# Performance work log

Measured on AMD Instinct MI355X. Metric: run time of the kernel, lower is better.

## Reference

```python
import jax, jax.numpy as jnp
import numpy as np
from jax import lax

BN_EPS = 1e-5


def _conv1d(h, w, b=None):
    # h: [B, Cin, L], w: [Cout, Cin, K], 'same' padding for odd K
    k = w.shape[-1]
    out = lax.conv_general_dilated(h, w, (1,), [(k // 2, k // 2)],
                                   dimension_numbers=('NCH', 'OIH', 'NCH'))
    if b is not None:
        out = out + b[None, :, None]
    return out


def _bn(h, gamma, beta):
    # eval-mode BatchNorm1d with running_mean=0, running_var=1
    return h * (gamma[None, :, None] / jnp.sqrt(1.0 + BN_EPS)) + beta[None, :, None]


def _encoder(h, cw, cb, rw, gammas, betas, aw, au):
    # h: [B, D, L] -> V: [B, C, F]
    t = jnp.tanh(_conv1d(h, cw, cb))
    t = _bn(t, gammas[0], betas[0])
    for i in range(rw.shape[0]):  # residual blocks
        t = jnp.tanh(_bn(_conv1d(t, rw[i]), gammas[i + 1], betas[i + 1]) + t)
    # label attention: w [A,F], u [C,A]
    Z = jnp.tanh(jnp.einsum('af,bfl->bal', aw, t))
    A = jax.nn.softmax(jnp.einsum('ca,bal->bcl', au, Z), axis=2)
    V = jnp.einsum('bfl,bcl->bcf', t, A)
    return V


def setup_inputs() -> dict:
    key = jax.random.key(0)
    ks = list(jax.random.split(key, 32))
    B, L, D, C, VOC, NE, N, E = 16, 4096, 256, 50, 50000, 20050, 512, 8192
    F, A, FFN = 100, 256, 128

    def rn(k, shape, s):
        return (jax.random.normal(k, shape, jnp.float32) * s).astype(jnp.float32)

    x = jax.random.randint(ks[0], (B, L), 0, VOC)
    attention_mask = jnp.ones((B, L), jnp.int32)
    nodes = jax.random.randint(ks[1], (B, N), 0, NE)
    src = jax.random.randint(ks[2], (B, E), 0, N)
    off = jax.random.randint(ks[3], (B, E), 1, N)
    dst = (src + off) % N  # guaranteed no self-loops
    edges = jnp.stack([src, dst], axis=1)  # [B, 2, E]

    inp = dict(x=x, attention_mask=attention_mask, nodes=nodes, edges=edges)
    inp['word_emb'] = rn(ks[4], (VOC, D), 0.02)
    inp['entity_emb'] = rn(ks[5], (NE, D), 0.02)
    i = 6
    for ksz in (3, 5, 9):
        inp[f'convw{ksz}'] = rn(ks[i], (F, D, ksz), (2.0 / (D * ksz)) ** 0.5); i += 1
        inp[f'convb{ksz}'] = jnp.zeros((F,), jnp.float32)
        inp[f'resw{ksz}'] = rn(ks[i], (2, F, F, ksz), (2.0 / (F * ksz)) ** 0.5); i += 1
    inp['bn_gamma'] = jnp.ones((3, 3, F), jnp.float32)
    inp['bn_beta'] = jnp.zeros((3, 3, F), jnp.float32)
    inp['attn_w'] = rn(ks[i], (3, A, F), 0.05); i += 1
    inp['attn_u'] = rn(ks[i], (3, C, A), 0.05); i += 1
    inp['gc1_w'] = rn(ks[i], (D, D), (1.0 / D) ** 0.5); i += 1
    inp['gc1_b'] = jnp.zeros((D,), jnp.float32)
    inp['gc2_w'] = rn(ks[i], (D, D), (1.0 / D) ** 0.5); i += 1
    inp['gc2_b'] = jnp.zeros((D,), jnp.float32)
    inp['fin1_w'] = rn(ks[i], (FFN, 3 * F + D), 0.05); i += 1
    inp['fin1_b'] = jnp.zeros((FFN,), jnp.float32)
    inp['fin2_w'] = rn(ks[i], (C, FFN), 0.05); i += 1
    inp['fin2_b'] = jnp.zeros((C,), jnp.float32)
    return inp


def reference(x, attention_mask, nodes, edges, word_emb, entity_emb,
              convw3, convb3, resw3, convw5, convb5, resw5, convw9, convb9, resw9,
              bn_gamma, bn_beta, attn_w, attn_u,
              gc1_w, gc1_b, gc2_w, gc2_b, fin1_w, fin1_b, fin2_w, fin2_b):
    C = fin2_b.shape[0]
    h = word_emb[x]                      # [B, L, D]
    h = jnp.transpose(h, (0, 2, 1))      # [B, D, L]

    Vs = []
    for i, (cw, cb, rw) in enumerate([(convw3, convb3, resw3),
                                      (convw5, convb5, resw5),
                                      (convw9, convb9, resw9)]):
        Vs.append(_encoder(h, cw, cb, rw, bn_gamma[i], bn_beta[i], attn_w[i], attn_u[i]))
    V = jnp.concatenate(Vs, axis=2)      # [B, C, 300]

    node_emb = entity_emb[nodes]         # [B, N, D]

    def per_graph(ne, ei):
        N = ne.shape[0]
        sl = jnp.arange(N)
        s = jnp.concatenate([ei[0], sl])  # GCNConv adds self-loops
        d = jnp.concatenate([ei[1], sl])
        deg = jax.ops.segment_sum(jnp.ones(s.shape[0], jnp.float32), d, num_segments=N)
        dinv = jnp.where(deg > 0, lax.rsqrt(deg), 0.0)
        norm = (dinv[s] * dinv[d])[:, None]

        def gconv(hh, W, b):
            return jax.ops.segment_sum((hh @ W.T)[s] * norm, d, num_segments=N) + b

        g = jax.nn.relu(gconv(ne, gc1_w, gc1_b))
        g = gconv(g, gc2_w, gc2_b)
        return g[:C]

    out_graphs = jax.vmap(per_graph)(node_emb, edges)  # [B, C, D]

    out = jnp.concatenate([out_graphs, V], axis=2)     # [B, C, D+300]
    hid = jax.nn.relu(jnp.einsum('bcf,hf->bch', out, fin1_w) + fin1_b)
    y_hat = jnp.sum(fin2_w[None] * hid, axis=2) + fin2_b  # [B, C]
    return y_hat
```

## Files before the change

kernel.cpp:

```cpp
#include <hip/hip_runtime.h>


#define CDIV(a,b) (((a)+(b)-1)/(b))

#define B_    16
#define L_    4096
#define D_    256
#define LP_   4112
#define POFF  8
#define F_    100
#define A_    256
#define C_    50
#define NN_   512
#define EE_   8192
#define ADJ_  8704
#define OC_   560

#define WFC1_STRIDE ((size_t)9*8*8*512)
#define WFRES_STRIDE ((size_t)9*4*8*512)
#define WFAW_STRIDE ((size_t)4*16*512)
#define WFAU_STRIDE ((size_t)8*4*512)

typedef unsigned short u16;
using short8  = __attribute__((ext_vector_type(8))) short;
using short4v = __attribute__((ext_vector_type(4))) short;
using f32x4   = __attribute__((ext_vector_type(4))) float;

__device__ __forceinline__ u16 f2b(float f){
    unsigned u = __float_as_uint(f);
    u += 0x7FFF + ((u >> 16) & 1);
    return (u16)(u >> 16);
}
__device__ __forceinline__ float b2f(u16 h){ return __uint_as_float(((unsigned)h) << 16); }

__global__ void fill_i_k(int* p, int n, int v){
    int i = blockIdx.x*256 + threadIdx.x; if (i < n) p[i] = v;
}
__global__ void zero_pads1_k(u16* p){
    int idx = blockIdx.x*256 + threadIdx.x;
    if (idx >= B_*16*128) return;
    int ch = idx & 127; int rest = idx >> 7;
    int pc = rest & 15; int b = rest >> 4;
    int col = (pc < 8) ? pc : (4096 + pc);
    p[((size_t)b*LP_ + col)*128 + ch] = 0;
}

__global__ __launch_bounds__(256) void embed1_k(const int* __restrict__ x,
                                                const float* __restrict__ emb,
                                                u16* __restrict__ hH){
    int b = blockIdx.y;
    int col = blockIdx.x*8 + (threadIdx.x >> 5);
    int cg  = (threadIdx.x & 31) * 8;
    size_t o = ((size_t)b*LP_ + col)*D_ + cg;
    int l = col - POFF;
    short8 h0;
    if (l < 0 || l >= L_){
        #pragma unroll
        for (int i = 0; i < 8; ++i) h0[i] = 0;
    } else {
        int tok = x[b*L_ + l];
        const float* s = emb + (size_t)tok*D_ + cg;
        #pragma unroll
        for (int i = 0; i < 8; ++i) h0[i] = (short)f2b(s[i]);
    }
    *(short8*)(hH + o) = h0;
}

__device__ __forceinline__ void pack_frag(const float* src, u16* dst,
                                          int M, int K, int kt, int nch, int MTtot, int idx){
    int i = idx & 7, lane = (idx >> 3) & 63, rest = idx >> 9;
    int mt = rest % MTtot, r2 = rest / MTtot;
    int cc = r2 % nch,  j = r2 / nch;
    int m  = mt*16 + (lane & 15);
    int ch = cc*32 + (lane >> 4)*8 + i;
    float v = (m < M && ch < K) ? src[((size_t)m*K + ch)*kt + j] : 0.f;
    dst[(size_t)rest*512 + lane*8 + i] = f2b(v);
}
__global__ void pack_conv1_k(const float* w3, const float* w5, const float* w9, u16* dst){
    int br = blockIdx.y;
    int k = (br == 0) ? 3 : (br == 1) ? 5 : 9;
    const float* s = (br == 0) ? w3 : (br == 1) ? w5 : w9;
    int idx = blockIdx.x*256 + threadIdx.x;
    if (idx < k*8*8*512) pack_frag(s, dst + (size_t)br*WFC1_STRIDE, F_, 256, k, 8, 8, idx);
}
__global__ void pack_res_k(const float* w3, const float* w5, const float* w9, u16* dst){
    int br = blockIdx.y, blk = blockIdx.z;
    int k = (br == 0) ? 3 : (br == 1) ? 5 : 9;
    const float* s = ((br == 0) ? w3 : (br == 1) ? w5 : w9) + (size_t)blk*F_*F_*k;
    int idx = blockIdx.x*256 + threadIdx.x;
    if (idx < k*4*8*512) pack_frag(s, dst + (size_t)(br*2 + blk)*WFRES_STRIDE, F_, F_, k, 4, 8, idx);
}
__global__ void pack_aw_k(const float* aw, u16* dst){
    int br = blockIdx.y;
    int idx = blockIdx.x*256 + threadIdx.x;
    if (idx < 4*16*512) pack_frag(aw + (size_t)br*A_*F_, dst + (size_t)br*WFAW_STRIDE, A_, F_, 1, 4, 16, idx);
}
__global__ void pack_au_k(const float* au, u16* dst){
    int br = blockIdx.y;
    int idx = blockIdx.x*256 + threadIdx.x;
    if (idx < 8*4*512) pack_frag(au + (size_t)br*C_*A_, dst + (size_t)br*WFAU_STRIDE, C_, A_, 1, 8, 4, idx);
}
__global__ void transpose_fin1_k(const float* __restrict__ src, float* __restrict__ dst){
    int idx = blockIdx.x*256 + threadIdx.x;
    if (idx >= OC_*128) return;
    int h = idx & 127, j = idx >> 7;
    dst[idx] = (j < 556) ? src[h*556 + j] : 0.f;
}

template<int KT, int MODE, int NCH>
__global__ __launch_bounds__(256) void conv_mfma_k(
    const u16* __restrict__ in, int CHp_in,
    const u16* __restrict__ wf,
    const float* __restrict__ bias, const float* __restrict__ gamma,
    const float* __restrict__ beta,
    u16* __restrict__ out, u16* __restrict__ outT)
{
    __shared__ short sm[12800];
    const int tid = threadIdx.x, lane = tid & 63;
    const int w = tid >> 6;
    const int q = lane >> 4, lr = lane & 15;
    const int n0 = blockIdx.x * 64;
    const int b  = blockIdx.y;
    const u16* inb = in + (size_t)b*LP_*CHp_in;

    f32x4 acc[2][4];
    #pragma unroll
    for (int t = 0; t < 2; ++t)
        #pragma unroll
        for (int n = 0; n < 4; ++n) acc[t][n] = (f32x4){0.f,0.f,0.f,0.f};

    constexpr int NPASS = NCH / 4;
    for (int pass = 0; pass < NPASS; ++pass){
        for (int idx = tid; idx < 1280; idx += 256){
            int cc = idx >> 8;
            cc = idx / 320;
            int e = idx - cc*320;
            int col = e >> 2, qq = e & 3;
            *(short8*)(sm + cc*3200 + col*40 + qq*8) =
                *(const short8*)(inb + (size_t)(n0 + col)*CHp_in + (pass*4 + cc)*32 + qq*8);
        }
        __syncthreads();
        auto fragPtr = [&](int it)->const u16*{
            int j = it >> 2, cc = it & 3;
            int rest = (j*NCH + pass*4 + cc)*8 + w*2;
            return wf + (size_t)rest*512 + lane*8;
        };
        short8 Ac0 = *(const short8*)(fragPtr(0));
        short8 Ac1 = *(const short8*)(fragPtr(0) + 512);
        #pragma unroll
        for (int it = 0; it < KT*4; ++it){
            short8 An0, An1;
            if (it + 1 < KT*4){
                const u16* fn = fragPtr(it+1);
                An0 = *(const short8*)(fn);
                An1 = *(const short8*)(fn + 512);
            }
            int j = it >> 2, cc = it & 3;
            int sc0 = 8 - (KT >> 1) + j + lr;
            short8 Bv[4];
            #pragma unroll
            for (int n = 0; n < 4; ++n)
                Bv[n] = *(const short8*)(sm + cc*3200 + (sc0 + n*16)*40 + q*8);
            #pragma unroll
            for (int n = 0; n < 4; ++n){
                acc[0][n] = __builtin_amdgcn_mfma_f32_16x16x32_bf16(Ac0, Bv[n], acc[0][n], 0,0,0);
                acc[1][n] = __builtin_amdgcn_mfma_f32_16x16x32_bf16(Ac1, Bv[n], acc[1][n], 0,0,0);
            }
            if (it + 1 < KT*4){ Ac0 = An0; Ac1 = An1; }
        }
        __syncthreads();
    }

    const float BNS = 0.9999950000374997f;
    for (int p = 0; p < 2; ++p){
        #pragma unroll
        for (int t = 0; t < 2; ++t){
            #pragma unroll
            for (int u = 0; u < 2; ++u){
                int n = p*2 + u;
                int mbase = w*32 + t*16 + q*4;
                int cl = u*16 + lr;
                int colg = n0 + n*16 + lr;
                float rsum[4] = {0.f,0.f,0.f,0.f};
                if (MODE == 1){
                    size_t ro = ((size_t)b*LP_ + POFF + colg)*CHp_in + mbase;
                    short4v rh = *(const short4v*)(in + ro);
                    #pragma unroll
                    for (int r = 0; r < 4; ++r) rsum[r] = b2f((u16)rh[r]);
                }
                short4v hv;
                #pragma unroll
                for (int r = 0; r < 4; ++r){
                    int mm = mbase + r;
                    float a = acc[t][n][r];
                    float v;
                    if (MODE == 0){
                        float bi=0.f, s=0.f, be=0.f;
                        if (mm < F_){ bi = bias[mm]; s = gamma[mm]*BNS; be = beta[mm]; }
                        v = tanhf(a + bi)*s + be;
                    } else {
                        float s=0.f, be=0.f;
                        if (mm < F_){ s = gamma[mm]*BNS; be = beta[mm]; }
                        v = tanhf(fmaf(a, s, be) + rsum[r]);
                    }
                    hv[r] = (short)f2b(v);
                }
                *(short4v*)(sm + cl*136 + mbase) = hv;
            }
        }
        __syncthreads();
        for (int idx = tid; idx < 512; idx += 256){
            int col = idx >> 4, q8 = idx & 15;
            short8 vv = *(const short8*)(sm + col*136 + q8*8);
            *(short8*)(out + ((size_t)b*LP_ + POFF + n0 + p*32 + col)*128 + q8*8) = vv;
        }
        if (outT){
            int f = tid & 127, half = tid >> 7;
            u16 vals[16];
            #pragma unroll
            for (int i = 0; i < 16; ++i) vals[i] = (u16)sm[(half*16 + i)*136 + f];
            short8 v0, v1;
            #pragma unroll
            for (int i = 0; i < 8; ++i){ v0[i] = (short)vals[i]; v1[i] = (short)vals[8+i]; }
            u16* dst = outT + ((size_t)b*128 + f)*L_ + n0 + p*32 + half*16;
            *(short8*)dst = v0;
            *(short8*)(dst + 8) = v1;
        }
        __syncthreads();
    }
}

__global__ __launch_bounds__(256) void attn_k(const u16* __restrict__ tpl,
                                              const u16* __restrict__ awf,
                                              const u16* __restrict__ auf,
                                              float* __restrict__ S){
    __shared__ short sm[17408];
    const int tid = threadIdx.x, lane = tid & 63;
    const int w = tid >> 6, wm = w >> 1, wn = w & 1;
    const int q = lane >> 4, lr = lane & 15;
    const int n0 = blockIdx.x * 128;
    const int b  = blockIdx.y;

    for (int idx = tid; idx < 2048; idx += 256){
        int col = idx >> 4, g = idx & 15;
        *(short8*)(sm + col*136 + g*8) =
            *(const short8*)(tpl + ((size_t)b*LP_ + POFF + n0 + col)*128 + g*8);
    }
    __syncthreads();

    f32x4 acc1[8][4];
    #pragma unroll
    for (int t = 0; t < 8; ++t)
        #pragma unroll
        for (int n = 0; n < 4; ++n) acc1[t][n] = (f32x4){0.f,0.f,0.f,0.f};
    for (int cc = 0; cc < 4; ++cc){
        short8 Af[8];
        const u16* fp = awf + (size_t)(cc*16 + wm*8)*512 + lane*8;
        #pragma unroll
        for (int t = 0; t < 8; ++t) Af[t] = *(const short8*)(fp + (size_t)t*512);
        short8 Bf[4];
        #pragma unroll
        for (int n = 0; n < 4; ++n)
            Bf[n] = *(const short8*)(sm + (wn*64 + n*16 + lr)*136 + cc*32 + q*8);
        #pragma unroll
        for (int t = 0; t < 8; ++t)
            #pragma unroll
            for (int n = 0; n < 4; ++n)
                acc1[t][n] = __builtin_amdgcn_mfma_f32_16x16x32_bf16(Af[t], Bf[n], acc1[t][n], 0,0,0);
    }
    __syncthreads();

    for (int p = 0; p < 2; ++p){
        if (wn == p){
            #pragma unroll
            for (int t = 0; t < 8; ++t){
                #pragma unroll
                for (int n = 0; n < 4; ++n){
                    int abase = wm*128 + t*16 + q*4;
                    int cl = n*16 + lr;
                    short4v zv;
                    #pragma unroll
                    for (int r = 0; r < 4; ++r) zv[r] = (short)f2b(tanhf(acc1[t][n][r]));
                    *(short4v*)(sm + cl*264 + abase) = zv;
                }
            }
        }
        __syncthreads();
        f32x4 acc2[4];
        #pragma unroll
        for (int t = 0; t < 4; ++t) acc2[t] = (f32x4){0.f,0.f,0.f,0.f};
        for (int cc = 0; cc < 8; ++cc){
            short8 Af2[4];
            const u16* fp2 = auf + (size_t)(cc*4)*512 + lane*8;
            #pragma unroll
            for (int t = 0; t < 4; ++t) Af2[t] = *(const short8*)(fp2 + (size_t)t*512);
            short8 Bf2 = *(const short8*)(sm + (w*16 + lr)*264 + cc*32 + q*8);
            #pragma unroll
            for (int t = 0; t < 4; ++t)
                acc2[t] = __builtin_amdgcn_mfma_f32_16x16x32_bf16(Af2[t], Bf2, acc2[t], 0,0,0);
        }
        #pragma unroll
        for (int t = 0; t < 4; ++t)
            #pragma unroll
            for (int r = 0; r < 4; ++r){
                int c = t*16 + q*4 + r;
                S[((size_t)b*64 + c)*L_ + n0 + p*64 + w*16 + lr] = acc2[t][r];
            }
        __syncthreads();
    }
}

__global__ __launch_bounds__(256) void softmax_k(float* __restrict__ S){
    int c = blockIdx.x, b = blockIdx.y, t = threadIdx.x;
    float* p = S + ((size_t)b*64 + c)*L_;
    __shared__ float sh[256];
    float mx = -1e30f;
    for (int j = t; j < L_; j += 256) mx = fmaxf(mx, p[j]);
    sh[t] = mx; __syncthreads();
    for (int o = 128; o > 0; o >>= 1){ if (t < o) sh[t] = fmaxf(sh[t], sh[t+o]); __syncthreads(); }
    float m = sh[0]; __syncthreads();
    float sum = 0.f;
    for (int j = t; j < L_; j += 256){ float e = expf(p[j] - m); p[j] = e; sum += e; }
    sh[t] = sum; __syncthreads();
    for (int o = 128; o > 0; o >>= 1){ if (t < o) sh[t] += sh[t+o]; __syncthreads(); }
    float inv = 1.0f / sh[0];
    for (int j = t; j < L_; j += 256) p[j] *= inv;
}

__global__ __launch_bounds__(256) void v_mfma_k(const u16* __restrict__ tT,
                                                const float* __restrict__ S,
                                                float* __restrict__ Vpart){
    int cx = blockIdx.x, b = blockIdx.y;
    int w = threadIdx.x >> 6, lane = threadIdx.x & 63;
    int q = lane >> 4, lr = lane & 15;
    int l0 = cx*128;
    f32x4 acc[7];
    #pragma unroll
    for (int mt = 0; mt < 7; ++mt) acc[mt] = (f32x4){0.f,0.f,0.f,0.f};
    const u16* tb = tT + (size_t)b*128*L_;
    const float* Sb = S + ((size_t)b*64 + w*16 + lr)*L_;
    #pragma unroll
    for (int kk = 0; kk < 4; ++kk){
        int l = l0 + kk*32 + q*8;
        float4 s0 = *(const float4*)(Sb + l);
        float4 s1 = *(const float4*)(Sb + l + 4);
        short8 Bf;
        Bf[0] = (short)f2b(s0.x); Bf[1] = (short)f2b(s0.y);
        Bf[2] = (short)f2b(s0.z); Bf[3] = (short)f2b(s0.w);
        Bf[4] = (short)f2b(s1.x); Bf[5] = (short)f2b(s1.y);
        Bf[6] = (short)f2b(s1.z); Bf[7] = (short)f2b(s1.w);
        #pragma unroll
        for (int mt = 0; mt < 7; ++mt){
            short8 Af = *(const short8*)(tb + (size_t)(mt*16 + lr)*L_ + l);
            acc[mt] = __builtin_amdgcn_mfma_f32_16x16x32_bf16(Af, Bf, acc[mt], 0,0,0);
        }
    }
    int c = w*16 + lr;
    if (c < C_){
        float* vp = Vpart + ((size_t)(b*64 + c)*32 + cx)*112;
        #pragma unroll
        for (int mt = 0; mt < 7; ++mt)
            *(f32x4*)(vp + mt*16 + q*4) = acc[mt];
    }
}

__global__ void reduce_v_k(const float* __restrict__ Vp, float* __restrict__ oc, int coloff){
    int idx = blockIdx.x*256 + threadIdx.x;
    if (idx >= B_*C_*F_) return;
    int f = idx % F_; int rest = idx / F_;
    int c = rest % C_; int b = rest / C_;
    const float* src = Vp + ((size_t)(b*64 + c)*32)*112 + f;
    float s = 0.f;
    #pragma unroll
    for (int cx = 0; cx < 32; ++cx) s += src[cx*112];
    oc[((size_t)b*C_ + c)*OC_ + 256 + coloff + f] = s;
}

__global__ void gather_nodes_k(const int* __restrict__ nodes, const float* __restrict__ emb,
                               float* __restrict__ ne){
    int idx = blockIdx.x*256 + threadIdx.x;
    if (idx >= B_*NN_*D_) return;
    int d = idx & 255, n = (idx >> 8) & 511, b = idx >> 17;
    ne[idx] = emb[(size_t)nodes[b*NN_ + n]*D_ + d];
}
__global__ void deg_count_k(const int* __restrict__ edges, int* __restrict__ deg){
    int idx = blockIdx.x*256 + threadIdx.x;
    if (idx >= B_*EE_) return;
    int b = idx >> 13, e = idx & (EE_-1);
    int dst = edges[b*2*EE_ + EE_ + e];
    atomicAdd(&deg[b*NN_ + dst], 1);
}
__global__ void dinv_k(const int* __restrict__ deg, float* __restrict__ dinv){
    int i = blockIdx.x*256 + threadIdx.x;
    if (i < B_*NN_) dinv[i] = 1.0f / sqrtf((float)deg[i]);
}
__global__ void scan_csr_k(const int* __restrict__ deg, int* __restrict__ rp, int* __restrict__ cur){
    int b = blockIdx.x, t = threadIdx.x;
    __shared__ int sh[NN_];
    int v = deg[b*NN_ + t];
    sh[t] = v; __syncthreads();
    for (int off = 1; off < NN_; off <<= 1){
        int x = (t >= off) ? sh[t-off] : 0;
        __syncthreads();
        sh[t] += x;
        __syncthreads();
    }
    int incl = sh[t], excl = incl - v;
    rp[b*513 + t] = excl;
    cur[b*NN_ + t] = excl;
    if (t == NN_-1) rp[b*513 + NN_] = incl;
}
__global__ void fill_csr_k(const int* __restrict__ edges, int* __restrict__ cur, int* __restrict__ adj){
    int e = blockIdx.x*256 + threadIdx.x, b = blockIdx.y;
    if (e >= ADJ_) return;
    int s, d;
    if (e < EE_){ s = edges[b*2*EE_ + e]; d = edges[b*2*EE_ + EE_ + e]; }
    else        { s = d = e - EE_; }
    int pos = atomicAdd(&cur[b*NN_ + d], 1);
    adj[b*ADJ_ + pos] = s;
}
__global__ __launch_bounds__(256) void gemm_nt_k(const float* __restrict__ A,
                                                 const float* __restrict__ W,
                                                 float* __restrict__ out){
    int b = blockIdx.z, n0 = blockIdx.x*64, i0 = blockIdx.y*64;
    __shared__ float aL[64][17], wL[64][17];
    int tid = threadIdx.x, tx = tid & 15, ty = tid >> 4;
    const float* Ab = A + (size_t)b*NN_*D_;
    float acc[4][4];
    #pragma unroll
    for (int r = 0; r < 4; ++r)
        #pragma unroll
        for (int i = 0; i < 4; ++i) acc[r][i] = 0.f;
    for (int j0 = 0; j0 < D_; j0 += 16){
        for (int idx = tid; idx < 1024; idx += 256){
            int r = idx >> 4, cc = idx & 15;
            aL[r][cc] = Ab[(size_t)(n0+r)*D_ + j0 + cc];
            wL[r][cc] = W[(size_t)(i0+r)*D_ + j0 + cc];
        }
        __syncthreads();
        #pragma unroll
        for (int kk = 0; kk < 16; ++kk){
            float av[4], wv[4];
            #pragma unroll
            for (int r = 0; r < 4; ++r) av[r] = aL[ty*4+r][kk];
            #pragma unroll
            for (int i = 0; i < 4; ++i) wv[i] = wL[tx*4+i][kk];
            #pragma unroll
            for (int r = 0; r < 4; ++r)
                #pragma unroll
                for (int i = 0; i < 4; ++i) acc[r][i] = fmaf(av[r], wv[i], acc[r][i]);
        }
        __syncthreads();
    }
    float* ob = out + (size_t)b*NN_*D_;
    #pragma unroll
    for (int r = 0; r < 4; ++r)
        #pragma unroll
        for (int i = 0; i < 4; ++i)
            ob[(size_t)(n0+ty*4+r)*D_ + i0+tx*4+i] = acc[r][i];
}
__global__ __launch_bounds__(256) void scatter_k(const float* __restrict__ xw,
                                                 const int* __restrict__ adj,
                                                 const int* __restrict__ rp,
                                                 const float* __restrict__ dinv,
                                                 const float* __restrict__ bias,
                                                 float* __restrict__ out,
                                                 int out_bs, int out_ld, int relu){
    int n = blockIdx.x, b = blockIdx.y, t = threadIdx.x;
    const int* rpb = rp + b*513;
    const int* adjb = adj + b*ADJ_;
    const float* xwb = xw + (size_t)b*NN_*D_;
    const float* dvb = dinv + b*NN_;
    int e0 = rpb[n], e1 = rpb[n+1];
    float acc = 0.f;
    for (int e = e0; e < e1; ++e){
        int s = adjb[e];
        acc = fmaf(xwb[(size_t)s*D_ + t], dvb[s], acc);
    }
    float v = fmaf(acc, dvb[n], bias[t]);
    if (relu) v = fmaxf(v, 0.f);
    out[(size_t)b*out_bs + (size_t)n*out_ld + t] = v;
}

__global__ __launch_bounds__(128) void final_k(const float* __restrict__ oc,
                                               const float* __restrict__ w1t,
                                               const float* __restrict__ b1,
                                               const float* __restrict__ w2,
                                               const float* __restrict__ b2,
                                               float* __restrict__ y){
    int c = blockIdx.x, b = blockIdx.y, h = threadIdx.x;
    __shared__ float row[OC_];
    __shared__ float red[128];
    const float* src = oc + ((size_t)b*C_ + c)*OC_;
    for (int j = h; j < OC_; j += 128) row[j] = src[j];
    __syncthreads();
    float acc = b1[h];
    #pragma unroll 8
    for (int j = 0; j < OC_; ++j) acc = fmaf(row[j], w1t[j*128 + h], acc);
    float hid = fmaxf(acc, 0.f);
    red[h] = hid * w2[c*128 + h];
    __syncthreads();
    for (int o = 64; o > 0; o >>= 1){ if (h < o) red[h] += red[h+o]; __syncthreads(); }
    if (h == 0) y[b*C_ + c] = red[0] + b2[c];
}

extern "C" void kernel_launch(void* const* d_in, const int* in_sizes, int n_in,
                              void* d_out, int out_size, void* d_ws, size_t ws_size,
                              hipStream_t stream){
    (void)in_sizes; (void)n_in; (void)out_size; (void)ws_size;
    const int*   x          = (const int*)d_in[0];
    const int*   nodes      = (const int*)d_in[2];
    const int*   edges      = (const int*)d_in[3];
    const float* word_emb   = (const float*)d_in[4];
    const float* entity_emb = (const float*)d_in[5];
    const float* convb[3]   = {(const float*)d_in[7], (const float*)d_in[10], (const float*)d_in[13]};
    const float* bn_gamma   = (const float*)d_in[15];
    const float* bn_beta    = (const float*)d_in[16];
    const float* gc1_w      = (const float*)d_in[19];
    const float* gc1_b      = (const float*)d_in[20];
    const float* gc2_w      = (const float*)d_in[21];
    const float* gc2_b      = (const float*)d_in[22];
    const float* fin1_w     = (const float*)d_in[23];
    const float* fin1_b     = (const float*)d_in[24];
    const float* fin2_w     = (const float*)d_in[25];
    const float* fin2_b     = (const float*)d_in[26];
    float* y = (float*)d_out;

    char* base = (char*)d_ws;
    size_t off = 0;
    auto alloc = [&](size_t elems, size_t esz) -> char* {
        char* p = base + off;
        off += ((elems*esz + 255) / 256) * 256;
        return p;
    };
    u16* hH  = (u16*)alloc((size_t)B_*LP_*D_, 2);
    u16* t0  = (u16*)alloc((size_t)B_*LP_*128, 2);
    u16* t1  = (u16*)alloc((size_t)B_*LP_*128, 2);
    u16* tT  = (u16*)alloc((size_t)B_*128*L_, 2);
    float* S     = (float*)alloc((size_t)B_*64*L_, 4);
    float* Vpart = (float*)alloc((size_t)B_*64*32*112, 4);
    float* ne   = (float*)alloc((size_t)B_*NN_*D_, 4);
    float* xw   = (float*)alloc((size_t)B_*NN_*D_, 4);
    float* g1   = (float*)alloc((size_t)B_*NN_*D_, 4);
    float* ocat = (float*)alloc((size_t)B_*C_*OC_, 4);
    u16* wfc1  = (u16*)alloc(3*WFC1_STRIDE, 2);
    u16* wfres = (u16*)alloc(6*WFRES_STRIDE, 2);
    u16* wfaw  = (u16*)alloc(3*WFAW_STRIDE, 2);
    u16* wfau  = (u16*)alloc(3*WFAU_STRIDE, 2);
    float* w1t   = (float*)alloc((size_t)OC_*128, 4);
    float* dinvp = (float*)alloc((size_t)B_*NN_, 4);
    int* deg = (int*)alloc((size_t)B_*NN_, 4);
    int* rpB = (int*)alloc((size_t)B_*513, 4);
    int* cur = (int*)alloc((size_t)B_*NN_, 4);
    int* adj = (int*)alloc((size_t)B_*ADJ_, 4);

    fill_i_k<<<CDIV(B_*NN_,256),256,0,stream>>>(deg, B_*NN_, 1);
    zero_pads1_k<<<CDIV(B_*16*128,256),256,0,stream>>>(t0);
    zero_pads1_k<<<CDIV(B_*16*128,256),256,0,stream>>>(t1);
    pack_conv1_k<<<dim3(CDIV(9*8*8*512,256),3),256,0,stream>>>(
        (const float*)d_in[6], (const float*)d_in[9], (const float*)d_in[12], wfc1);
    pack_res_k<<<dim3(CDIV(9*4*8*512,256),3,2),256,0,stream>>>(
        (const float*)d_in[8], (const float*)d_in[11], (const float*)d_in[14], wfres);
    pack_aw_k<<<dim3(CDIV(4*16*512,256),3),256,0,stream>>>((const float*)d_in[17], wfaw);
    pack_au_k<<<dim3(CDIV(8*4*512,256),3),256,0,stream>>>((const float*)d_in[18], wfau);

    embed1_k<<<dim3(LP_/8, B_),256,0,stream>>>(x, word_emb, hH);

    gather_nodes_k<<<CDIV(B_*NN_*D_,256),256,0,stream>>>(nodes, entity_emb, ne);
    deg_count_k<<<CDIV(B_*EE_,256),256,0,stream>>>(edges, deg);
    dinv_k<<<CDIV(B_*NN_,256),256,0,stream>>>(deg, dinvp);
    scan_csr_k<<<B_,NN_,0,stream>>>(deg, rpB, cur);
    fill_csr_k<<<dim3(CDIV(ADJ_,256),B_),256,0,stream>>>(edges, cur, adj);
    gemm_nt_k<<<dim3(NN_/64, D_/64, B_),256,0,stream>>>(ne, gc1_w, xw);
    scatter_k<<<dim3(NN_,B_),256,0,stream>>>(xw, adj, rpB, dinvp, gc1_b, g1, NN_*D_, D_, 1);
    gemm_nt_k<<<dim3(NN_/64, D_/64, B_),256,0,stream>>>(g1, gc2_w, xw);
    scatter_k<<<dim3(C_,B_),256,0,stream>>>(xw, adj, rpB, dinvp, gc2_b, ocat, C_*OC_, OC_, 0);

    dim3 gc(64, B_), ga(32, B_);
    for (int br = 0; br < 3; ++br){
        const float* gam = bn_gamma + br*300;
        const float* bet = bn_beta + br*300;
        const u16* wc = wfc1 + (size_t)br*WFC1_STRIDE;
        const u16* wr1 = wfres + (size_t)(br*2+0)*WFRES_STRIDE;
        const u16* wr2 = wfres + (size_t)(br*2+1)*WFRES_STRIDE;
        if (br == 0){
            conv_mfma_k<3,0,8><<<gc,256,0,stream>>>(hH,256, wc, convb[br],gam,bet, t0, nullptr);
            conv_mfma_k<3,1,4><<<gc,256,0,stream>>>(t0,128, wr1, nullptr,gam+100,bet+100, t1, nullptr);
            conv_mfma_k<3,1,4><<<gc,256,0,stream>>>(t1,128, wr2, nullptr,gam+200,bet+200, t0, tT);
        } else if (br == 1){
            conv_mfma_k<5,0,8><<<gc,256,0,stream>>>(hH,256, wc, convb[br],gam,bet, t0, nullptr);
            conv_mfma_k<5,1,4><<<gc,256,0,stream>>>(t0,128, wr1, nullptr,gam+100,bet+100, t1, nullptr);
            conv_mfma_k<5,1,4><<<gc,256,0,stream>>>(t1,128, wr2, nullptr,gam+200,bet+200, t0, tT);
        } else {
            conv_mfma_k<9,0,8><<<gc,256,0,stream>>>(hH,256, wc, convb[br],gam,bet, t0, nullptr);
            conv_mfma_k<9,1,4><<<gc,256,0,stream>>>(t0,128, wr1, nullptr,gam+100,bet+100, t1, nullptr);
            conv_mfma_k<9,1,4><<<gc,256,0,stream>>>(t1,128, wr2, nullptr,gam+200,bet+200, t0, tT);
        }
        attn_k<<<ga,256,0,stream>>>(t0, wfaw + (size_t)br*WFAW_STRIDE,
                                    wfau + (size_t)br*WFAU_STRIDE, S);
        softmax_k<<<dim3(C_,B_),256,0,stream>>>(S);
        v_mfma_k<<<dim3(32, B_),256,0,stream>>>(tT, S, Vpart);
        reduce_v_k<<<CDIV(B_*C_*F_,256),256,0,stream>>>(Vpart, ocat, br*100);
    }

    transpose_fin1_k<<<CDIV(OC_*128,256),256,0,stream>>>(fin1_w, w1t);
    final_k<<<dim3(C_,B_),128,0,stream>>>(ocat, w1t, fin1_b, fin2_w, fin2_b, y);
}
```

Before: 827.4 us.

## Batch three encoder branches into single launches and store attention scores in bf16

Merges the three conv branches (kernel sizes 3/5/9) into one grid dimension per stage, so each conv, attention, softmax, V and reduce stage runs as one launch over all branches instead of three serialized launches. Kernel size becomes a runtime value, so the inner MFMA loop is no longer fully unrolled. Attention scores are stored as bf16 to halve softmax and V traffic, and V partials use 256-wide chunks to halve the reduction. The workspace is reorganised with aliasing of hH onto t1 and Vpart onto the graph buffers, which adds an extra pad zeroing after the first conv and lowers softmax precision.

Result: faster. 708.4 us (-14.4%).

```diff
diff --git a/kernel.cpp b/kernel.cpp
--- a/kernel.cpp
+++ b/kernel.cpp
@@ -16,6 +16,11 @@
 #define ADJ_  8704
 #define OC_   560
 
+#define PLANE ((size_t)B_*LP_*128)
+#define TTS   ((size_t)B_*128*L_)
+#define SST   ((size_t)B_*64*L_)
+#define VPS   ((size_t)B_*64*16*112)
+
 #define WFC1_STRIDE ((size_t)9*8*8*512)
 #define WFRES_STRIDE ((size_t)9*4*8*512)
 #define WFAW_STRIDE ((size_t)4*16*512)
@@ -36,13 +41,14 @@
 __global__ void fill_i_k(int* p, int n, int v){
     int i = blockIdx.x*256 + threadIdx.x; if (i < n) p[i] = v;
 }
-__global__ void zero_pads1_k(u16* p){
-    int idx = blockIdx.x*256 + threadIdx.x;
-    if (idx >= B_*16*128) return;
+__global__ void zero_pads3_k(u16* p){
+    int idx = blockIdx.x*256 + threadIdx.x;
+    if (idx >= 3*B_*16*128) return;
     int ch = idx & 127; int rest = idx >> 7;
-    int pc = rest & 15; int b = rest >> 4;
+    int pc = rest & 15; rest >>= 4;
+    int b = rest & 15;  int br = rest >> 4;
     int col = (pc < 8) ? pc : (4096 + pc);
-    p[((size_t)b*LP_ + col)*128 + ch] = 0;
+    p[(size_t)br*PLANE + ((size_t)b*LP_ + col)*128 + ch] = 0;
 }
 
 __global__ __launch_bounds__(256) void embed1_k(const int* __restrict__ x,
@@ -107,13 +113,14 @@
     dst[idx] = (j < 556) ? src[h*556 + j] : 0.f;
 }
 
-template<int KT, int MODE, int NCH>
+template<int MODE, int NCH>
 __global__ __launch_bounds__(256) void conv_mfma_k(
-    const u16* __restrict__ in, int CHp_in,
-    const u16* __restrict__ wf,
-    const float* __restrict__ bias, const float* __restrict__ gamma,
-    const float* __restrict__ beta,
-    u16* __restrict__ out, u16* __restrict__ outT)
+    const u16* __restrict__ in_base, int CHp_in, long in_bs,
+    const u16* __restrict__ wf_base, long wf_bs,
+    const float* __restrict__ bias0, const float* __restrict__ bias1,
+    const float* __restrict__ bias2,
+    const float* __restrict__ gamma_base, const float* __restrict__ beta_base, int layeroff,
+    u16* __restrict__ out_base, u16* __restrict__ outT_base)
 {
     __shared__ short sm[12800];
     const int tid = threadIdx.x, lane = tid & 63;
@@ -121,6 +128,15 @@
     const int q = lane >> 4, lr = lane & 15;
     const int n0 = blockIdx.x * 64;
     const int b  = blockIdx.y;
+    const int br = blockIdx.z;
+    const int kt = (br == 0) ? 3 : (br == 1) ? 5 : 9;
+    const u16* in = in_base + (size_t)br*in_bs;
+    const u16* wf = wf_base + (size_t)br*wf_bs;
+    const float* bias = (MODE == 0) ? ((br == 0) ? bias0 : (br == 1) ? bias1 : bias2) : nullptr;
+    const float* gamma = gamma_base + br*300 + layeroff;
+    const float* beta  = beta_base  + br*300 + layeroff;
+    u16* out  = out_base + (size_t)br*PLANE;
+    u16* outT = outT_base ? (outT_base + (size_t)br*TTS) : nullptr;
     const u16* inb = in + (size_t)b*LP_*CHp_in;
 
     f32x4 acc[2][4];
@@ -132,8 +148,7 @@
     constexpr int NPASS = NCH / 4;
     for (int pass = 0; pass < NPASS; ++pass){
         for (int idx = tid; idx < 1280; idx += 256){
-            int cc = idx >> 8;
-            cc = idx / 320;
+            int cc = idx / 320;
             int e = idx - cc*320;
             int col = e >> 2, qq = e & 3;
             *(short8*)(sm + cc*3200 + col*40 + qq*8) =
@@ -145,18 +160,18 @@
             int rest = (j*NCH + pass*4 + cc)*8 + w*2;
             return wf + (size_t)rest*512 + lane*8;
         };
+        const int kt4 = kt*4;
         short8 Ac0 = *(const short8*)(fragPtr(0));
         short8 Ac1 = *(const short8*)(fragPtr(0) + 512);
-        #pragma unroll
-        for (int it = 0; it < KT*4; ++it){
+        for (int it = 0; it < kt4; ++it){
             short8 An0, An1;
-            if (it + 1 < KT*4){
+            if (it + 1 < kt4){
                 const u16* fn = fragPtr(it+1);
                 An0 = *(const short8*)(fn);
                 An1 = *(const short8*)(fn + 512);
             }
             int j = it >> 2, cc = it & 3;
-            int sc0 = 8 - (KT >> 1) + j + lr;
+            int sc0 = 8 - (kt >> 1) + j + lr;
             short8 Bv[4];
             #pragma unroll
             for (int n = 0; n < 4; ++n)
@@ -166,7 +181,7 @@
                 acc[0][n] = __builtin_amdgcn_mfma_f32_16x16x32_bf16(Ac0, Bv[n], acc[0][n], 0,0,0);
                 acc[1][n] = __builtin_amdgcn_mfma_f32_16x16x32_bf16(Ac1, Bv[n], acc[1][n], 0,0,0);
             }
-            if (it + 1 < KT*4){ Ac0 = An0; Ac1 = An1; }
+            if (it + 1 < kt4){ Ac0 = An0; Ac1 = An1; }
         }
         __syncthreads();
     }
@@ -230,16 +245,21 @@
     }
 }
 
-__global__ __launch_bounds__(256) void attn_k(const u16* __restrict__ tpl,
-                                              const u16* __restrict__ awf,
-                                              const u16* __restrict__ auf,
-                                              float* __restrict__ S){
+__global__ __launch_bounds__(256) void attn_k(const u16* __restrict__ t_base,
+                                              const u16* __restrict__ awf_base,
+                                              const u16* __restrict__ auf_base,
+                                              u16* __restrict__ S_base){
     __shared__ short sm[17408];
     const int tid = threadIdx.x, lane = tid & 63;
     const int w = tid >> 6, wm = w >> 1, wn = w & 1;
     const int q = lane >> 4, lr = lane & 15;
     const int n0 = blockIdx.x * 128;
     const int b  = blockIdx.y;
+    const int br = blockIdx.z;
+    const u16* tpl = t_base + (size_t)br*PLANE;
+    const u16* awf = awf_base + (size_t)br*WFAW_STRIDE;
+    const u16* auf = auf_base + (size_t)br*WFAU_STRIDE;
+    u16* S = S_base + (size_t)br*SST;
 
     for (int idx = tid; idx < 2048; idx += 256){
         int col = idx >> 4, g = idx & 15;
@@ -304,51 +324,45 @@
             #pragma unroll
             for (int r = 0; r < 4; ++r){
                 int c = t*16 + q*4 + r;
-                S[((size_t)b*64 + c)*L_ + n0 + p*64 + w*16 + lr] = acc2[t][r];
+                S[((size_t)b*64 + c)*L_ + n0 + p*64 + w*16 + lr] = f2b(acc2[t][r]);
             }
         __syncthreads();
     }
 }
 
-__global__ __launch_bounds__(256) void softmax_k(float* __restrict__ S){
-    int c = blockIdx.x, b = blockIdx.y, t = threadIdx.x;
-    float* p = S + ((size_t)b*64 + c)*L_;
+__global__ __launch_bounds__(256) void softmax_k(u16* __restrict__ S){
+    int c = blockIdx.x, b = blockIdx.y, br = blockIdx.z, t = threadIdx.x;
+    u16* p = S + (size_t)br*SST + ((size_t)b*64 + c)*L_;
     __shared__ float sh[256];
     float mx = -1e30f;
-    for (int j = t; j < L_; j += 256) mx = fmaxf(mx, p[j]);
+    for (int j = t; j < L_; j += 256) mx = fmaxf(mx, b2f(p[j]));
     sh[t] = mx; __syncthreads();
     for (int o = 128; o > 0; o >>= 1){ if (t < o) sh[t] = fmaxf(sh[t], sh[t+o]); __syncthreads(); }
     float m = sh[0]; __syncthreads();
     float sum = 0.f;
-    for (int j = t; j < L_; j += 256){ float e = expf(p[j] - m); p[j] = e; sum += e; }
+    for (int j = t; j < L_; j += 256){ float e = expf(b2f(p[j]) - m); p[j] = f2b(e); sum += e; }
     sh[t] = sum; __syncthreads();
     for (int o = 128; o > 0; o >>= 1){ if (t < o) sh[t] += sh[t+o]; __syncthreads(); }
     float inv = 1.0f / sh[0];
-    for (int j = t; j < L_; j += 256) p[j] *= inv;
-}
-
-__global__ __launch_bounds__(256) void v_mfma_k(const u16* __restrict__ tT,
-                                                const float* __restrict__ S,
-                                                float* __restrict__ Vpart){
-    int cx = blockIdx.x, b = blockIdx.y;
+    for (int j = t; j < L_; j += 256) p[j] = f2b(b2f(p[j]) * inv);
+}
+
+__global__ __launch_bounds__(256) void v_mfma_k(const u16* __restrict__ tT_base,
+                                                const u16* __restrict__ S_base,
+                                                float* __restrict__ Vp_base){
+    int cx = blockIdx.x, b = blockIdx.y, br = blockIdx.z;
     int w = threadIdx.x >> 6, lane = threadIdx.x & 63;
     int q = lane >> 4, lr = lane & 15;
-    int l0 = cx*128;
+    int l0 = cx*256;
     f32x4 acc[7];
     #pragma unroll
     for (int mt = 0; mt < 7; ++mt) acc[mt] = (f32x4){0.f,0.f,0.f,0.f};
-    const u16* tb = tT + (size_t)b*128*L_;
-    const float* Sb = S + ((size_t)b*64 + w*16 + lr)*L_;
+    const u16* tb = tT_base + (size_t)br*TTS + (size_t)b*128*L_;
+    const u16* Sb = S_base + (size_t)br*SST + ((size_t)b*64 + w*16 + lr)*L_;
     #pragma unroll
-    for (int kk = 0; kk < 4; ++kk){
+    for (int kk = 0; kk < 8; ++kk){
         int l = l0 + kk*32 + q*8;
-        float4 s0 = *(const float4*)(Sb + l);
-        float4 s1 = *(const float4*)(Sb + l + 4);
-        short8 Bf;
-        Bf[0] = (short)f2b(s0.x); Bf[1] = (short)f2b(s0.y);
-        Bf[2] = (short)f2b(s0.z); Bf[3] = (short)f2b(s0.w);
-        Bf[4] = (short)f2b(s1.x); Bf[5] = (short)f2b(s1.y);
-        Bf[6] = (short)f2b(s1.z); Bf[7] = (short)f2b(s1.w);
+        short8 Bf = *(const short8*)(Sb + l);
         #pragma unroll
         for (int mt = 0; mt < 7; ++mt){
             short8 Af = *(const short8*)(tb + (size_t)(mt*16 + lr)*L_ + l);
@@ -357,23 +371,24 @@
     }
     int c = w*16 + lr;
     if (c < C_){
-        float* vp = Vpart + ((size_t)(b*64 + c)*32 + cx)*112;
+        float* vp = Vp_base + (size_t)br*VPS + ((size_t)(b*64 + c)*16 + cx)*112;
         #pragma unroll
         for (int mt = 0; mt < 7; ++mt)
             *(f32x4*)(vp + mt*16 + q*4) = acc[mt];
     }
 }
 
-__global__ void reduce_v_k(const float* __restrict__ Vp, float* __restrict__ oc, int coloff){
-    int idx = blockIdx.x*256 + threadIdx.x;
-    if (idx >= B_*C_*F_) return;
+__global__ void reduce_v_k(const float* __restrict__ Vp, float* __restrict__ oc){
+    int idx = blockIdx.x*256 + threadIdx.x;
+    if (idx >= 3*B_*C_*F_) return;
     int f = idx % F_; int rest = idx / F_;
-    int c = rest % C_; int b = rest / C_;
-    const float* src = Vp + ((size_t)(b*64 + c)*32)*112 + f;
+    int c = rest % C_; rest /= C_;
+    int b = rest % B_; int br = rest / B_;
+    const float* src = Vp + (size_t)br*VPS + ((size_t)(b*64 + c)*16)*112 + f;
     float s = 0.f;
     #pragma unroll
-    for (int cx = 0; cx < 32; ++cx) s += src[cx*112];
-    oc[((size_t)b*C_ + c)*OC_ + 256 + coloff + f] = s;
+    for (int cx = 0; cx < 16; ++cx) s += src[cx*112];
+    oc[((size_t)b*C_ + c)*OC_ + 256 + br*100 + f] = s;
 }
 
 __global__ void gather_nodes_k(const int* __restrict__ nodes, const float* __restrict__ emb,
@@ -513,7 +528,6 @@
     const int*   edges      = (const int*)d_in[3];
     const float* word_emb   = (const float*)d_in[4];
     const float* entity_emb = (const float*)d_in[5];
-    const float* convb[3]   = {(const float*)d_in[7], (const float*)d_in[10], (const float*)d_in[13]};
     const float* bn_gamma   = (const float*)d_in[15];
     const float* bn_beta    = (const float*)d_in[16];
     const float* gc1_w      = (const float*)d_in[19];
@@ -528,35 +542,35 @@
 
     char* base = (char*)d_ws;
     size_t off = 0;
-    auto alloc = [&](size_t elems, size_t esz) -> char* {
+    auto alloc = [&](size_t bytes) -> char* {
         char* p = base + off;
-        off += ((elems*esz + 255) / 256) * 256;
+        off += ((bytes + 255) / 256) * 256;
         return p;
     };
-    u16* hH  = (u16*)alloc((size_t)B_*LP_*D_, 2);
-    u16* t0  = (u16*)alloc((size_t)B_*LP_*128, 2);
-    u16* t1  = (u16*)alloc((size_t)B_*LP_*128, 2);
-    u16* tT  = (u16*)alloc((size_t)B_*128*L_, 2);
-    float* S     = (float*)alloc((size_t)B_*64*L_, 4);
-    float* Vpart = (float*)alloc((size_t)B_*64*32*112, 4);
-    float* ne   = (float*)alloc((size_t)B_*NN_*D_, 4);
-    float* xw   = (float*)alloc((size_t)B_*NN_*D_, 4);
-    float* g1   = (float*)alloc((size_t)B_*NN_*D_, 4);
-    float* ocat = (float*)alloc((size_t)B_*C_*OC_, 4);
-    u16* wfc1  = (u16*)alloc(3*WFC1_STRIDE, 2);
-    u16* wfres = (u16*)alloc(6*WFRES_STRIDE, 2);
-    u16* wfaw  = (u16*)alloc(3*WFAW_STRIDE, 2);
-    u16* wfau  = (u16*)alloc(3*WFAU_STRIDE, 2);
-    float* w1t   = (float*)alloc((size_t)OC_*128, 4);
-    float* dinvp = (float*)alloc((size_t)B_*NN_, 4);
-    int* deg = (int*)alloc((size_t)B_*NN_, 4);
-    int* rpB = (int*)alloc((size_t)B_*513, 4);
-    int* cur = (int*)alloc((size_t)B_*NN_, 4);
-    int* adj = (int*)alloc((size_t)B_*ADJ_, 4);
+    u16* t0 = (u16*)alloc(3*PLANE*2);
+    u16* t1 = (u16*)alloc(3*PLANE*2);
+    u16* hH = t1;
+    u16* tT = (u16*)alloc(3*TTS*2);
+    u16* S  = (u16*)alloc(3*SST*2);
+    char* G = alloc((size_t)3*B_*NN_*D_*4);
+    float* ne = (float*)G;
+    float* xw = ne + (size_t)B_*NN_*D_;
+    float* g1 = xw + (size_t)B_*NN_*D_;
+    float* Vpart = (float*)G;
+    float* ocat = (float*)alloc((size_t)B_*C_*OC_*4);
+    u16* wfc1  = (u16*)alloc(3*WFC1_STRIDE*2);
+    u16* wfres = (u16*)alloc(6*WFRES_STRIDE*2);
+    u16* wfaw  = (u16*)alloc(3*WFAW_STRIDE*2);
+    u16* wfau  = (u16*)alloc(3*WFAU_STRIDE*2);
+    float* w1t   = (float*)alloc((size_t)OC_*128*4);
+    float* dinvp = (float*)alloc((size_t)B_*NN_*4);
+    int* deg = (int*)alloc((size_t)B_*NN_*4);
+    int* rpB = (int*)alloc((size_t)B_*513*4);
+    int* cur = (int*)alloc((size_t)B_*NN_*4);
+    int* adj = (int*)alloc((size_t)B_*ADJ_*4);
 
     fill_i_k<<<CDIV(B_*NN_,256),256,0,stream>>>(deg, B_*NN_, 1);
-    zero_pads1_k<<<CDIV(B_*16*128,256),256,0,stream>>>(t0);
-    zero_pads1_k<<<CDIV(B_*16*128,256),256,0,stream>>>(t1);
+    zero_pads3_k<<<CDIV(3*B_*16*128,256),256,0,stream>>>(t0);
     pack_conv1_k<<<dim3(CDIV(9*8*8*512,256),3),256,0,stream>>>(
         (const float*)d_in[6], (const float*)d_in[9], (const float*)d_in[12], wfc1);
     pack_res_k<<<dim3(CDIV(9*4*8*512,256),3,2),256,0,stream>>>(
@@ -576,32 +590,24 @@
     gemm_nt_k<<<dim3(NN_/64, D_/64, B_),256,0,stream>>>(g1, gc2_w, xw);
     scatter_k<<<dim3(C_,B_),256,0,stream>>>(xw, adj, rpB, dinvp, gc2_b, ocat, C_*OC_, OC_, 0);
 
-    dim3 gc(64, B_), ga(32, B_);
-    for (int br = 0; br < 3; ++br){
-        const float* gam = bn_gamma + br*300;
-        const float* bet = bn_beta + br*300;
-        const u16* wc = wfc1 + (size_t)br*WFC1_STRIDE;
-        const u16* wr1 = wfres + (size_t)(br*2+0)*WFRES_STRIDE;
-        const u16* wr2 = wfres + (size_t)(br*2+1)*WFRES_STRIDE;
-        if (br == 0){
-            conv_mfma_k<3,0,8><<<gc,256,0,stream>>>(hH,256, wc, convb[br],gam,bet, t0, nullptr);
-            conv_mfma_k<3,1,4><<<gc,256,0,stream>>>(t0,128, wr1, nullptr,gam+100,bet+100, t1, nullptr);
-            conv_mfma_k<3,1,4><<<gc,256,0,stream>>>(t1,128, wr2, nullptr,gam+200,bet+200, t0, tT);
-        } else if (br == 1){
-            conv_mfma_k<5,0,8><<<gc,256,0,stream>>>(hH,256, wc, convb[br],gam,bet, t0, nullptr);
-            conv_mfma_k<5,1,4><<<gc,256,0,stream>>>(t0,128, wr1, nullptr,gam+100,bet+100, t1, nullptr);
-            conv_mfma_k<5,1,4><<<gc,256,0,stream>>>(t1,128, wr2, nullptr,gam+200,bet+200, t0, tT);
-        } else {
-            conv_mfma_k<9,0,8><<<gc,256,0,stream>>>(hH,256, wc, convb[br],gam,bet, t0, nullptr);
-            conv_mfma_k<9,1,4><<<gc,256,0,stream>>>(t0,128, wr1, nullptr,gam+100,bet+100, t1, nullptr);
-            conv_mfma_k<9,1,4><<<gc,256,0,stream>>>(t1,128, wr2, nullptr,gam+200,bet+200, t0, tT);
-        }
-        attn_k<<<ga,256,0,stream>>>(t0, wfaw + (size_t)br*WFAW_STRIDE,
-                                    wfau + (size_t)br*WFAU_STRIDE, S);
-        softmax_k<<<dim3(C_,B_),256,0,stream>>>(S);
-        v_mfma_k<<<dim3(32, B_),256,0,stream>>>(tT, S, Vpart);
-        reduce_v_k<<<CDIV(B_*C_*F_,256),256,0,stream>>>(Vpart, ocat, br*100);
-    }
+    dim3 gc(64, B_, 3), ga(32, B_, 3);
+    conv_mfma_k<0,8><<<gc,256,0,stream>>>(hH, 256, 0,
+        wfc1, (long)WFC1_STRIDE,
+        (const float*)d_in[7], (const float*)d_in[10], (const float*)d_in[13],
+        bn_gamma, bn_beta, 0, t0, nullptr);
+    zero_pads3_k<<<CDIV(3*B_*16*128,256),256,0,stream>>>(t1);
+    conv_mfma_k<1,4><<<gc,256,0,stream>>>(t0, 128, (long)PLANE,
+        wfres, (long)(2*WFRES_STRIDE),
+        nullptr, nullptr, nullptr,
+        bn_gamma, bn_beta, 100, t1, nullptr);
+    conv_mfma_k<1,4><<<gc,256,0,stream>>>(t1, 128, (long)PLANE,
+        wfres + WFRES_STRIDE, (long)(2*WFRES_STRIDE),
+        nullptr, nullptr, nullptr,
+        bn_gamma, bn_beta, 200, t0, tT);
+    attn_k<<<ga,256,0,stream>>>(t0, wfaw, wfau, S);
+    softmax_k<<<dim3(C_,B_,3),256,0,stream>>>(S);
+    v_mfma_k<<<dim3(16,B_,3),256,0,stream>>>(tT, S, Vpart);
+    reduce_v_k<<<CDIV(3*B_*C_*F_,256),256,0,stream>>>(Vpart, ocat);
 
     transpose_fin1_k<<<CDIV(OC_*128,256),256,0,stream>>>(fin1_w, w1t);
     final_k<<<dim3(C_,B_),128,0,stream>>>(ocat, w1t, fin1_b, fin2_w, fin2_b, y);
```
